# Kernel tuning notes

Measured on AMD Instinct MI355X. Metric: run time of the kernel, lower is better.

Reference implementation:

```python
import jax, jax.numpy as jnp
import numpy as np

D = 256
H = 8
HD = D // H
LN_EPS = 1e-5


def setup_inputs() -> dict:
    key = jax.random.key(0)
    ks = jax.random.split(key, 20)
    N = 768
    s = lambda *sh: 1.0 / np.sqrt(sh[-1])
    inp = {
        "features": jax.random.normal(ks[0], (N, D), jnp.float32),
        "boxes": jax.random.uniform(ks[1], (N, 4), jnp.float32),
        # MultiheadAttention params (torch layout: [out, in])
        "in_proj_w": jax.random.normal(ks[2], (3 * D, D), jnp.float32) * s(D),
        "in_proj_b": jnp.zeros((3 * D,), jnp.float32),
        "out_proj_w": jax.random.normal(ks[3], (D, D), jnp.float32) * s(D),
        "out_proj_b": jnp.zeros((D,), jnp.float32),
        # similarity_net params
        "w1": jax.random.normal(ks[4], (256, 3 * D + 3), jnp.float32) * s(3 * D + 3),
        "b1": jnp.zeros((256,), jnp.float32),
        "ln_g": jnp.ones((256,), jnp.float32),
        "ln_b": jnp.zeros((256,), jnp.float32),
        "w2": jax.random.normal(ks[5], (128, 256), jnp.float32) * s(256),
        "b2": jnp.zeros((128,), jnp.float32),
        "w3": jax.random.normal(ks[6], (64, 128), jnp.float32) * s(128),
        "b3": jnp.zeros((64,), jnp.float32),
        "w4": jax.random.normal(ks[7], (32, 64), jnp.float32) * s(64),
        "b4": jnp.zeros((32,), jnp.float32),
        "w5": jax.random.normal(ks[8], (1, 32), jnp.float32) * s(32),
        "b5": jnp.zeros((1,), jnp.float32),
    }
    return inp


def _mha(x, in_w, in_b, out_w, out_b):
    # x: [N, D]; torch nn.MultiheadAttention self-attention (eval mode)
    N = x.shape[0]
    qkv = x @ in_w.T + in_b                      # [N, 3D]
    q, k, v = jnp.split(qkv, 3, axis=-1)
    q = q.reshape(N, H, HD).transpose(1, 0, 2)   # [H, N, HD]
    k = k.reshape(N, H, HD).transpose(1, 0, 2)
    v = v.reshape(N, H, HD).transpose(1, 0, 2)
    scores = jnp.einsum("hnd,hmd->hnm", q, k) / np.sqrt(HD)
    attn = jax.nn.softmax(scores, axis=-1)
    o = jnp.einsum("hnm,hmd->hnd", attn, v)      # [H, N, HD]
    o = o.transpose(1, 0, 2).reshape(N, D)
    return o @ out_w.T + out_b


def reference(features, boxes, in_proj_w, in_proj_b, out_proj_w, out_proj_b,
              w1, b1, ln_g, ln_b, w2, b2, w3, b3, w4, b4, w5, b5):
    N = features.shape[0]
    att = _mha(features, in_proj_w, in_proj_b, out_proj_w, out_proj_b)  # [N, D]

    fi = jnp.broadcast_to(att[:, None, :], (N, N, D))
    fj = jnp.broadcast_to(att[None, :, :], (N, N, D))
    bi = boxes[:, None, :]
    bj = boxes[None, :, :]
    x_dist = jnp.abs(bi[:, :, 0] - bj[:, :, 0])
    y_diff = bi[:, :, 1] - bj[:, :, 1]
    spatial = jnp.stack([x_dist, jnp.abs(y_diff), y_diff], axis=-1)    # [N, N, 3]
    pairs = jnp.concatenate([fi, fj, fi * fj, spatial], axis=-1)       # [N, N, 3D+3]

    h = jax.nn.relu(pairs @ w1.T + b1)
    mu = jnp.mean(h, axis=-1, keepdims=True)
    var = jnp.var(h, axis=-1, keepdims=True)
    h = (h - mu) / jnp.sqrt(var + LN_EPS) * ln_g + ln_b
    h = jax.nn.relu(h @ w2.T + b2)
    h = jax.nn.relu(h @ w3.T + b3)
    h = jax.nn.relu(h @ w4.T + b4)
    logits = (h @ w5.T + b5)[..., 0]                                   # [N, N]

    eye = jnp.eye(N, dtype=logits.dtype)
    return logits * (1.0 - eye) - 1e9 * eye
```

## Files before the change

kernel.cpp:

```cpp
#include <hip/hip_runtime.h>


typedef __attribute__((ext_vector_type(8))) __bf16 bf16x8;
typedef __attribute__((ext_vector_type(4))) float f32x4;

__device__ __forceinline__ float bf2f(unsigned short u) {
    return __uint_as_float(((unsigned int)u) << 16);
}
__device__ __forceinline__ unsigned short f2bf(float f) {
    union { __bf16 b; unsigned short u; } cv;
    cv.b = (__bf16)f;
    return cv.u;
}
__device__ __forceinline__ int pk4_fp8(float a, float b, float c, float d) {
    int w = __builtin_amdgcn_cvt_pk_fp8_f32(a, b, 0, false);
    w = __builtin_amdgcn_cvt_pk_fp8_f32(c, d, w, true);
    return w;
}
__device__ __forceinline__ unsigned char f2fp8(float v) {
    return (unsigned char)(__builtin_amdgcn_cvt_pk_fp8_f32(v, 0.f, 0, false) & 0xff);
}

__global__ __launch_bounds__(256) void pack_all(
    const float* __restrict__ features, const float* __restrict__ in_proj_w,
    const float* __restrict__ out_proj_w, const float* __restrict__ w1,
    const float* __restrict__ w2, const float* __restrict__ w3,
    const float* __restrict__ w4, const float* __restrict__ b1,
    const float* __restrict__ ln_g, const float* __restrict__ ln_b,
    const float* __restrict__ b2, const float* __restrict__ out_proj_b,
    unsigned short* __restrict__ featb, unsigned short* __restrict__ inWb,
    unsigned short* __restrict__ WcatB, unsigned short* __restrict__ outWTb,
    unsigned short* __restrict__ wABb,
    unsigned char* __restrict__ w1c_f8, unsigned char* __restrict__ w2g_f8,
    unsigned char* __restrict__ w3_f8, unsigned char* __restrict__ w4_f8,
    float* __restrict__ bias768, float* __restrict__ c1, float* __restrict__ c2,
    float* __restrict__ biasZ)
{
    int t = blockIdx.x * 256 + threadIdx.x;
    if (t < 196608) {
        featb[t] = f2bf(features[t]);
    } else if (t < 393216) {
        int u = t - 196608; inWb[u] = f2bf(in_proj_w[u]);
    } else if (t < 458752) {
        int u = t - 393216; WcatB[u] = f2bf(out_proj_w[u]);
    } else if (t < 524288) {
        int u = t - 458752; int e = u >> 8, d = u & 255;
        outWTb[u] = f2bf(out_proj_w[d * 256 + e]);
    } else if (t < 655360) {
        int u = t - 524288; int n = u >> 8, k = u & 255;
        float v = (n < 256) ? w1[n * 771 + k] : w1[(n - 256) * 771 + 256 + k];
        wABb[u] = f2bf(v);
    } else if (t < 729088) {
        int u = t - 655360;
        int e = u & 7, lane = (u >> 3) & 63, f = u >> 9;
        int l15 = lane & 15, quad = lane >> 4;
        int mt = f & 15, kc = f >> 4;
        int o = mt * 16 + l15, k = kc * 32 + quad * 8 + e;
        float v;
        if (k < 256)            v = w1[o * 771 + 512 + k];
        else if (k < 259)       v = w1[o * 771 + 768 + (k - 256)];
        else                    v = 0.f;
        w1c_f8[u] = f2fp8(v);
    } else if (t < 761856) {
        int u = t - 729088;
        int e = u & 7, lane = (u >> 3) & 63, f = u >> 9;
        int l15 = lane & 15, quad = lane >> 4;
        int mt = f & 7, kc = f >> 3;
        int o = mt * 16 + l15, k = kc * 32 + quad * 8 + e;
        w2g_f8[u] = f2fp8(w2[o * 256 + k] * ln_g[k]);
    } else if (t < 770048) {
        int u = t - 761856;
        int e = u & 7, lane = (u >> 3) & 63, f = u >> 9;
        int l15 = lane & 15, quad = lane >> 4;
        int mt = f & 3, kc = f >> 2;
        int o = mt * 16 + l15, k = kc * 32 + quad * 8 + e;
        w3_f8[u] = f2fp8(w3[o * 128 + k]);
    } else if (t < 772096) {
        int u = t - 770048;
        int e = u & 7, lane = (u >> 3) & 63, f = u >> 9;
        int l15 = lane & 15, quad = lane >> 4;
        int mt = f & 1, kc = f >> 1;
        int o = mt * 16 + l15, k = kc * 32 + quad * 8 + e;
        w4_f8[u] = f2fp8(w4[o * 64 + k]);
    } else if (t < 772864) {
        int n = t - 772096;
        if (n < 256) bias768[n] = out_proj_b[n];
        else {
            int m = n - 256;
            float s = 0.f;
            for (int d = 0; d < 256; d += 4) {
                float4 ob = *reinterpret_cast<const float4*>(&out_proj_b[d]);
                const float* wr = (m < 256) ? &w1[m * 771 + d]
                                            : &w1[(m - 256) * 771 + 256 + d];
                float4 w = *reinterpret_cast<const float4*>(wr);
                s += ob.x * w.x + ob.y * w.y + ob.z * w.z + ob.w * w.w;
            }
            bias768[n] = s + ((m < 256) ? b1[m] : 0.f);
        }
    } else if (t < 772992) {
        int p = t - 772864;
        float s2 = 0.f, s1 = 0.f;
        for (int k = 0; k < 256; k += 4) {
            float4 w = *reinterpret_cast<const float4*>(&w2[p * 256 + k]);
            float4 g = *reinterpret_cast<const float4*>(&ln_g[k]);
            float4 lb = *reinterpret_cast<const float4*>(&ln_b[k]);
            s2 += g.x * w.x + g.y * w.y + g.z * w.z + g.w * w.w;
            s1 += lb.x * w.x + lb.y * w.y + lb.z * w.z + lb.w * w.w;
        }
        c2[p] = s2;
        c1[p] = s1 + b2[p];
    } else if (t < 773248) {
        biasZ[t - 772992] = 0.f;
    }
}

__global__ __launch_bounds__(256) void gemm_bf(
    const unsigned short* __restrict__ A, const unsigned short* __restrict__ W,
    const float* __restrict__ bias, float* __restrict__ Cf,
    unsigned short* __restrict__ Cbf, unsigned short* __restrict__ Vt,
    int N, int K, int ldc, int tcol0)
{
    const int wv = threadIdx.x >> 6, lane = threadIdx.x & 63;
    const int l15 = lane & 15, quad = lane >> 4;
    const int row0 = blockIdx.x * 64 + wv * 16;
    const int col0 = blockIdx.y * 64;
    f32x4 acc[4] = {};
    for (int kc = 0; kc < (K >> 5); ++kc) {
        bf16x8 a = *reinterpret_cast<const bf16x8*>(&A[(row0 + l15) * K + kc * 32 + quad * 8]);
#pragma unroll
        for (int ct = 0; ct < 4; ++ct) {
            bf16x8 b = *reinterpret_cast<const bf16x8*>(&W[(col0 + ct * 16 + l15) * K + kc * 32 + quad * 8]);
            acc[ct] = __builtin_amdgcn_mfma_f32_16x16x32_bf16(a, b, acc[ct], 0, 0, 0);
        }
    }
#pragma unroll
    for (int ct = 0; ct < 4; ++ct)
#pragma unroll
        for (int r = 0; r < 4; ++r) {
            int row = row0 + quad * 4 + r, col = col0 + ct * 16 + l15;
            float v = acc[ct][r] + bias[col];
            if (Vt && col >= tcol0) {
                Vt[(col - tcol0) * 768 + row] = f2bf(v);
            } else {
                if (Cf)  Cf[row * ldc + col] = v;
                if (Cbf) Cbf[row * ldc + col] = f2bf(v);
            }
        }
}

__global__ __launch_bounds__(256) void gemm_attab(
    const unsigned short* __restrict__ A, const unsigned short* __restrict__ W,
    const float* __restrict__ bias, float* __restrict__ att,
    unsigned short* __restrict__ attb, float* __restrict__ AB)
{
    const int wv = threadIdx.x >> 6, lane = threadIdx.x & 63;
    const int l15 = lane & 15, quad = lane >> 4;
    const int row0 = blockIdx.x * 64 + wv * 16;
    const int col0 = blockIdx.y * 64;
    f32x4 acc[4] = {};
    for (int kc = 0; kc < 8; ++kc) {
        bf16x8 a = *reinterpret_cast<const bf16x8*>(&A[(row0 + l15) * 256 + kc * 32 + quad * 8]);
#pragma unroll
        for (int ct = 0; ct < 4; ++ct) {
            bf16x8 b = *reinterpret_cast<const bf16x8*>(&W[(col0 + ct * 16 + l15) * 256 + kc * 32 + quad * 8]);
            acc[ct] = __builtin_amdgcn_mfma_f32_16x16x32_bf16(a, b, acc[ct], 0, 0, 0);
        }
    }
#pragma unroll
    for (int ct = 0; ct < 4; ++ct)
#pragma unroll
        for (int r = 0; r < 4; ++r) {
            int row = row0 + quad * 4 + r, col = col0 + ct * 16 + l15;
            float v = acc[ct][r] + bias[col];
            if (col < 256) {
                att[row * 256 + col] = v;
                attb[row * 256 + col] = f2bf(v);
            } else {
                AB[row * 512 + (col - 256)] = v;
            }
        }
}

#define SP 776

__global__ __launch_bounds__(256) void attn_mfma(
    const unsigned short* __restrict__ qkvb, const unsigned short* __restrict__ Vt,
    unsigned short* __restrict__ Obf)
{
    __shared__ __align__(16) unsigned short smS[64 * SP];
    const int h = blockIdx.x, q0 = blockIdx.y * 64, hb = h * 32;
    const int tid = threadIdx.x, wave = tid >> 6, lane = tid & 63;
    const int l15 = lane & 15, quad = lane >> 4;

    bf16x8 af[4];
#pragma unroll
    for (int mt = 0; mt < 4; ++mt)
        af[mt] = *reinterpret_cast<const bf16x8*>(&qkvb[(q0 + mt * 16 + l15) * 768 + hb + quad * 8]);
#pragma unroll
    for (int ct = 0; ct < 12; ++ct) {
        int n0 = wave * 192 + ct * 16;
        bf16x8 b = *reinterpret_cast<const bf16x8*>(&qkvb[(n0 + l15) * 768 + 256 + hb + quad * 8]);
#pragma unroll
        for (int mt = 0; mt < 4; ++mt) {
            f32x4 c = {};
            c = __builtin_amdgcn_mfma_f32_16x16x32_bf16(af[mt], b, c, 0, 0, 0);
#pragma unroll
            for (int r = 0; r < 4; ++r)
                smS[(mt * 16 + quad * 4 + r) * SP + n0 + l15] =
                    f2bf(c[r] * 0.17677669529663689f);
        }
    }
    __syncthreads();

    {
        const int row = tid >> 2, part = tid & 3;
        unsigned short* rp = &smS[row * SP + part * 192];
        float mx = -3.0e38f;
#pragma unroll
        for (int c8 = 0; c8 < 24; ++c8) {
            uint4 v = *reinterpret_cast<const uint4*>(&rp[c8 * 8]);
            const unsigned short* pe = reinterpret_cast<const unsigned short*>(&v);
#pragma unroll
            for (int e = 0; e < 8; ++e) mx = fmaxf(mx, bf2f(pe[e]));
        }
        mx = fmaxf(mx, __shfl_xor(mx, 1, 64));
        mx = fmaxf(mx, __shfl_xor(mx, 2, 64));
        float ls = 0.f;
#pragma unroll
        for (int c8 = 0; c8 < 24; ++c8) {
            uint4 v = *reinterpret_cast<const uint4*>(&rp[c8 * 8]);
            const unsigned short* pe = reinterpret_cast<const unsigned short*>(&v);
            unsigned short o8[8];
#pragma unroll
            for (int e = 0; e < 8; ++e) {
                float ev = __expf(bf2f(pe[e]) - mx);
                ls += ev;
                o8[e] = f2bf(ev);
            }
            *reinterpret_cast<uint4*>(&rp[c8 * 8]) = *reinterpret_cast<const uint4*>(o8);
        }
        ls += __shfl_xor(ls, 1, 64);
        ls += __shfl_xor(ls, 2, 64);
        float inv = 1.0f / ls;
#pragma unroll
        for (int c8 = 0; c8 < 24; ++c8) {
            uint4 v = *reinterpret_cast<const uint4*>(&rp[c8 * 8]);
            const unsigned short* pe = reinterpret_cast<const unsigned short*>(&v);
            unsigned short o8[8];
#pragma unroll
            for (int e = 0; e < 8; ++e) o8[e] = f2bf(bf2f(pe[e]) * inv);
            *reinterpret_cast<uint4*>(&rp[c8 * 8]) = *reinterpret_cast<const uint4*>(o8);
        }
    }
    f32x4 accp[2] = {};
    for (int kc = 0; kc < 24; ++kc) {
        bf16x8 a = *reinterpret_cast<const bf16x8*>(&smS[(wave * 16 + l15) * SP + kc * 32 + quad * 8]);
#pragma unroll
        for (int ct = 0; ct < 2; ++ct) {
            bf16x8 b = *reinterpret_cast<const bf16x8*>(&Vt[(hb + ct * 16 + l15) * 768 + kc * 32 + quad * 8]);
            accp[ct] = __builtin_amdgcn_mfma_f32_16x16x32_bf16(a, b, accp[ct], 0, 0, 0);
        }
    }
#pragma unroll
    for (int ct = 0; ct < 2; ++ct)
#pragma unroll
        for (int r = 0; r < 4; ++r) {
            int row = q0 + wave * 16 + quad * 4 + r;
            Obf[row * 256 + hb + ct * 16 + l15] = f2bf(accp[ct][r]);
        }
}

#define S1 296
#define S2 136
#define S3 72

__global__ __launch_bounds__(256, 4) void pair_mlp(
    const float* __restrict__ att, const unsigned short* __restrict__ attb,
    const float* __restrict__ AB,
    const unsigned char* __restrict__ w1c_f8, const unsigned char* __restrict__ w2g_f8,
    const unsigned char* __restrict__ w3_f8, const unsigned char* __restrict__ w4_f8,
    const float* __restrict__ boxes,
    const float* __restrict__ c1, const float* __restrict__ c2,
    const float* __restrict__ b3, const float* __restrict__ b4,
    const float* __restrict__ w5, const float* __restrict__ b5,
    float* __restrict__ out)
{
    __shared__ __align__(16) unsigned char smH[64 * S1];
    __shared__ float s_psum[64][4], s_pssq[64][4];
    __shared__ float s_mu[64], s_rs[64];
    __shared__ float s_l5[64][2];

    const int i    = blockIdx.x;
    const int j0   = blockIdx.y * 64;
    const int tid  = threadIdx.x;
    const int wave = tid >> 6;
    const int lane = tid & 63;
    const int l15  = lane & 15;
    const int quad = lane >> 4;

    {
        const int g = tid & 63;
        float4 fi4 = *reinterpret_cast<const float4*>(&att[i * 256 + g * 4]);
#pragma unroll
        for (int it = 0; it < 16; ++it) {
            int r = (tid >> 6) + it * 4;
            uint2 aj = *reinterpret_cast<const uint2*>(&attb[(j0 + r) * 256 + g * 4]);
            float a0 = __uint_as_float(aj.x << 16);
            float a1 = __uint_as_float(aj.x & 0xffff0000u);
            float a2 = __uint_as_float(aj.y << 16);
            float a3 = __uint_as_float(aj.y & 0xffff0000u);
            *reinterpret_cast<int*>(&smH[r * S1 + g * 4]) =
                pk4_fp8(a0 * fi4.x, a1 * fi4.y, a2 * fi4.z, a3 * fi4.w);
        }
    }
    if (tid < 64) {
        int j = j0 + tid;
        float xd = fabsf(boxes[i * 4 + 0] - boxes[j * 4 + 0]);
        float yd = boxes[i * 4 + 1] - boxes[j * 4 + 1];
        *reinterpret_cast<int*>(&smH[tid * S1 + 256]) = pk4_fp8(xd, fabsf(yd), yd, 0.f);
        *reinterpret_cast<int*>(&smH[tid * S1 + 260]) = 0;
        *reinterpret_cast<long long*>(&smH[tid * S1 + 264]) = 0;
        *reinterpret_cast<long long*>(&smH[tid * S1 + 272]) = 0;
        *reinterpret_cast<long long*>(&smH[tid * S1 + 280]) = 0;
    }
    __syncthreads();

    f32x4 acc1[4][4] = {};
    for (int kc = 0; kc < 9; ++kc) {
        long long a[4];
#pragma unroll
        for (int mt = 0; mt < 4; ++mt)
            a[mt] = *reinterpret_cast<const long long*>(&w1c_f8[((kc * 16 + wave * 4 + mt) * 64 + lane) * 8]);
#pragma unroll
        for (int nt = 0; nt < 4; ++nt) {
            long long b = *reinterpret_cast<const long long*>(&smH[(nt * 16 + l15) * S1 + kc * 32 + quad * 8]);
#pragma unroll
            for (int mt = 0; mt < 4; ++mt)
                acc1[mt][nt] = __builtin_amdgcn_mfma_f32_16x16x32_fp8_fp8(a[mt], b, acc1[mt][nt], 0, 0, 0);
        }
    }

    const int o0 = wave * 64;
    float vsum[4] = {}, vssq[4] = {};
#pragma unroll
    for (int mt = 0; mt < 4; ++mt) {
        int o = o0 + mt * 16 + quad * 4;
        float4 Ai = *reinterpret_cast<const float4*>(&AB[i * 512 + o]);
        float AiA[4] = {Ai.x, Ai.y, Ai.z, Ai.w};
#pragma unroll
        for (int nt = 0; nt < 4; ++nt) {
            int j = nt * 16 + l15;
            float4 Bj = *reinterpret_cast<const float4*>(&AB[(j0 + j) * 512 + 256 + o]);
            float BjA[4] = {Bj.x, Bj.y, Bj.z, Bj.w};
#pragma unroll
            for (int r = 0; r < 4; ++r) {
                float v = fmaxf(acc1[mt][nt][r] + AiA[r] + BjA[r], 0.f);
                acc1[mt][nt][r] = v;
                vsum[nt] += v; vssq[nt] += v * v;
            }
        }
    }
#pragma unroll
    for (int nt = 0; nt < 4; ++nt) {
        vsum[nt] += __shfl_xor(vsum[nt], 16, 64);
        vsum[nt] += __shfl_xor(vsum[nt], 32, 64);
        vssq[nt] += __shfl_xor(vssq[nt], 16, 64);
        vssq[nt] += __shfl_xor(vssq[nt], 32, 64);
    }
    if (quad == 0)
#pragma unroll
        for (int nt = 0; nt < 4; ++nt) {
            s_psum[nt * 16 + l15][wave] = vsum[nt];
            s_pssq[nt * 16 + l15][wave] = vssq[nt];
        }
    __syncthreads();
#pragma unroll
    for (int mt = 0; mt < 4; ++mt) {
        int o = o0 + mt * 16 + quad * 4;
#pragma unroll
        for (int nt = 0; nt < 4; ++nt) {
            int j = nt * 16 + l15;
            *reinterpret_cast<int*>(&smH[j * S1 + o]) =
                pk4_fp8(acc1[mt][nt][0], acc1[mt][nt][1], acc1[mt][nt][2], acc1[mt][nt][3]);
        }
    }
    if (wave == 0) {
        int j = lane;
        float sm = (s_psum[j][0] + s_psum[j][1] + s_psum[j][2] + s_psum[j][3]) * (1.0f / 256.0f);
        float sq = (s_pssq[j][0] + s_pssq[j][1] + s_pssq[j][2] + s_pssq[j][3]) * (1.0f / 256.0f);
        s_mu[j] = sm;
        s_rs[j] = rsqrtf(sq - sm * sm + 1e-5f);
    }
    __syncthreads();

    f32x4 acc2[2][4] = {};
    for (int kc = 0; kc < 8; ++kc) {
        long long a[2];
#pragma unroll
        for (int mt = 0; mt < 2; ++mt)
            a[mt] = *reinterpret_cast<const long long*>(&w2g_f8[((kc * 8 + wave * 2 + mt) * 64 + lane) * 8]);
#pragma unroll
        for (int nt = 0; nt < 4; ++nt) {
            long long b = *reinterpret_cast<const long long*>(&smH[(nt * 16 + l15) * S1 + kc * 32 + quad * 8]);
#pragma unroll
            for (int mt = 0; mt < 2; ++mt)
                acc2[mt][nt] = __builtin_amdgcn_mfma_f32_16x16x32_fp8_fp8(a[mt], b, acc2[mt][nt], 0, 0, 0);
        }
    }
    __syncthreads();
#pragma unroll
    for (int mt = 0; mt < 2; ++mt) {
        int p = wave * 32 + mt * 16 + quad * 4;
        float4 C1 = *reinterpret_cast<const float4*>(&c1[p]);
        float4 C2 = *reinterpret_cast<const float4*>(&c2[p]);
        float C1A[4] = {C1.x, C1.y, C1.z, C1.w};
        float C2A[4] = {C2.x, C2.y, C2.z, C2.w};
#pragma unroll
        for (int nt = 0; nt < 4; ++nt) {
            int j = nt * 16 + l15;
            float mu = s_mu[j], rs = s_rs[j];
            float vv[4];
#pragma unroll
            for (int r = 0; r < 4; ++r)
                vv[r] = fmaxf(rs * (acc2[mt][nt][r] - mu * C2A[r]) + C1A[r], 0.f);
            *reinterpret_cast<int*>(&smH[j * S2 + p]) = pk4_fp8(vv[0], vv[1], vv[2], vv[3]);
        }
    }
    __syncthreads();

    f32x4 acc3[4] = {};
    for (int kc = 0; kc < 4; ++kc) {
        long long a = *reinterpret_cast<const long long*>(&w3_f8[((kc * 4 + wave) * 64 + lane) * 8]);
#pragma unroll
        for (int nt = 0; nt < 4; ++nt) {
            long long b = *reinterpret_cast<const long long*>(&smH[(nt * 16 + l15) * S2 + kc * 32 + quad * 8]);
            acc3[nt] = __builtin_amdgcn_mfma_f32_16x16x32_fp8_fp8(a, b, acc3[nt], 0, 0, 0);
        }
    }
    __syncthreads();
    {
        int q = wave * 16 + quad * 4;
        float4 B3 = *reinterpret_cast<const float4*>(&b3[q]);
        float B3A[4] = {B3.x, B3.y, B3.z, B3.w};
#pragma unroll
        for (int nt = 0; nt < 4; ++nt) {
            int j = nt * 16 + l15;
            float vv[4];
#pragma unroll
            for (int r = 0; r < 4; ++r)
                vv[r] = fmaxf(acc3[nt][r] + B3A[r], 0.f);
            *reinterpret_cast<int*>(&smH[j * S3 + q]) = pk4_fp8(vv[0], vv[1], vv[2], vv[3]);
        }
    }
    __syncthreads();

    const int mt4 = wave & 1;
    const int jh  = wave >> 1;
    f32x4 acc4[2] = {};
#pragma unroll
    for (int kc = 0; kc < 2; ++kc) {
        long long a = *reinterpret_cast<const long long*>(&w4_f8[((kc * 2 + mt4) * 64 + lane) * 8]);
#pragma unroll
        for (int nt = 0; nt < 2; ++nt) {
            int j = jh * 32 + nt * 16 + l15;
            long long b = *reinterpret_cast<const long long*>(&smH[j * S3 + kc * 32 + quad * 8]);
            acc4[nt] = __builtin_amdgcn_mfma_f32_16x16x32_fp8_fp8(a, b, acc4[nt], 0, 0, 0);
        }
    }
    {
        int o4 = mt4 * 16 + quad * 4;
        float4 B4 = *reinterpret_cast<const float4*>(&b4[o4]);
        float4 W5 = *reinterpret_cast<const float4*>(&w5[o4]);
        float B4A[4] = {B4.x, B4.y, B4.z, B4.w};
        float W5A[4] = {W5.x, W5.y, W5.z, W5.w};
#pragma unroll
        for (int nt = 0; nt < 2; ++nt) {
            float part = 0.f;
#pragma unroll
            for (int r = 0; r < 4; ++r)
                part += fmaxf(acc4[nt][r] + B4A[r], 0.f) * W5A[r];
            part += __shfl_xor(part, 16, 64);
            part += __shfl_xor(part, 32, 64);
            if (quad == 0)
                s_l5[jh * 32 + nt * 16 + l15][mt4] = part;
        }
    }
    __syncthreads();
    if (tid < 64) {
        int j = j0 + tid;
        float v = s_l5[tid][0] + s_l5[tid][1] + b5[0];
        out[i * 768 + j] = (j == i) ? -1.0e9f : v;
    }
}

extern "C" void kernel_launch(void* const* d_in, const int* in_sizes, int n_in,
                              void* d_out, int out_size, void* d_ws, size_t ws_size,
                              hipStream_t stream)
{
    const float* features   = (const float*)d_in[0];
    const float* boxes      = (const float*)d_in[1];
    const float* in_proj_w  = (const float*)d_in[2];
    const float* in_proj_b  = (const float*)d_in[3];
    const float* out_proj_w = (const float*)d_in[4];
    const float* out_proj_b = (const float*)d_in[5];
    const float* w1  = (const float*)d_in[6];
    const float* b1  = (const float*)d_in[7];
    const float* ln_g = (const float*)d_in[8];
    const float* ln_b = (const float*)d_in[9];
    const float* w2  = (const float*)d_in[10];
    const float* b2  = (const float*)d_in[11];
    const float* w3  = (const float*)d_in[12];
    const float* b3  = (const float*)d_in[13];
    const float* w4  = (const float*)d_in[14];
    const float* b4  = (const float*)d_in[15];
    const float* w5  = (const float*)d_in[16];
    const float* b5  = (const float*)d_in[17];
    float* out = (float*)d_out;

    char* p = (char*)d_ws;
    unsigned short* qkvb  = (unsigned short*)p; p += 768 * 768 * 2;
    unsigned short* Vt    = (unsigned short*)p; p += 256 * 768 * 2;
    unsigned short* Obf   = (unsigned short*)p; p += 768 * 256 * 2;
    unsigned short* attb  = (unsigned short*)p; p += 768 * 256 * 2;
    float* att = (float*)p; p += 768 * 256 * 4;
    float* AB  = (float*)p; p += 768 * 512 * 4;
    unsigned short* featb  = (unsigned short*)p; p += 196608 * 2;
    unsigned short* inWb   = (unsigned short*)p; p += 196608 * 2;
    unsigned short* WcatB  = (unsigned short*)p; p += 196608 * 2;
    unsigned short* outWTb = (unsigned short*)p; p += 65536 * 2;
    unsigned short* wABb   = (unsigned short*)p; p += 131072 * 2;
    unsigned char* w1c_f8  = (unsigned char*)p; p += 73728;
    unsigned char* w2g_f8  = (unsigned char*)p; p += 32768;
    unsigned char* w3_f8   = (unsigned char*)p; p += 8192;
    unsigned char* w4_f8   = (unsigned char*)p; p += 2048;
    float* bias768 = (float*)p; p += 768 * 4;
    float* c1v     = (float*)p; p += 128 * 4;
    float* c2v     = (float*)p; p += 128 * 4;
    float* biasZ   = (float*)p; p += 256 * 4;

    pack_all<<<dim3(3021), dim3(256), 0, stream>>>(features, in_proj_w,
        out_proj_w, w1, w2, w3, w4, b1, ln_g, ln_b, b2, out_proj_b,
        featb, inWb, WcatB, outWTb, wABb, w1c_f8, w2g_f8, w3_f8, w4_f8,
        bias768, c1v, c2v, biasZ);
    gemm_bf<<<dim3(8, 4), dim3(256), 0, stream>>>(wABb, outWTb, biasZ,
        (float*)nullptr, WcatB + 65536, (unsigned short*)nullptr, 256, 256, 256, 1 << 30);
    gemm_bf<<<dim3(12, 12), dim3(256), 0, stream>>>(featb, inWb, in_proj_b,
        (float*)nullptr, qkvb, Vt, 768, 256, 768, 512);
    attn_mfma<<<dim3(8, 12), dim3(256), 0, stream>>>(qkvb, Vt, Obf);
    gemm_attab<<<dim3(12, 12), dim3(256), 0, stream>>>(Obf, WcatB, bias768,
        att, attb, AB);
    pair_mlp<<<dim3(768, 12), dim3(256), 0, stream>>>(att, attb, AB,
        w1c_f8, w2g_f8, w3_f8, w4_f8, boxes, c1v, c2v,
        b3, b4, w5, b5, out);
}
```

Baseline: 304.7 us.

## Use 32x32x16 fp8 MFMA for pair MLP layers 1-2 and split attention blocks

The first two pair-MLP GEMMs move from 16x16x32 to 32x32x16 fp8 MFMA instructions, and the w1/w2 fp8 weight packing is re-laid out to match the 32-row fragment layout. The goal is fewer MFMA issues and fewer LDS B-fragment loads per output. Layers 2 and 3 now get their own shared buffers (smH2, smH3), which removes one barrier at the cost of extra LDS per block, and that may lower occupancy. Attention blocks are halved to 32 query rows, doubling the grid so more CUs are busy, with an added barrier before the PV product.

```diff
diff --git a/kernel.cpp b/kernel.cpp
--- a/kernel.cpp
+++ b/kernel.cpp
@@ -3,6 +3,7 @@
 
 typedef __attribute__((ext_vector_type(8))) __bf16 bf16x8;
 typedef __attribute__((ext_vector_type(4))) float f32x4;
+typedef __attribute__((ext_vector_type(16))) float f32x16;
 
 __device__ __forceinline__ float bf2f(unsigned short u) {
     return __uint_as_float(((unsigned int)u) << 16);
@@ -53,9 +54,9 @@
     } else if (t < 729088) {
         int u = t - 655360;
         int e = u & 7, lane = (u >> 3) & 63, f = u >> 9;
-        int l15 = lane & 15, quad = lane >> 4;
-        int mt = f & 15, kc = f >> 4;
-        int o = mt * 16 + l15, k = kc * 32 + quad * 8 + e;
+        int ot = f & 7, k16 = f >> 3;
+        int o = ot * 32 + (lane & 31);
+        int k = k16 * 16 + ((lane >> 5) & 1) * 8 + e;
         float v;
         if (k < 256)            v = w1[o * 771 + 512 + k];
         else if (k < 259)       v = w1[o * 771 + 768 + (k - 256)];
@@ -64,10 +65,10 @@
     } else if (t < 761856) {
         int u = t - 729088;
         int e = u & 7, lane = (u >> 3) & 63, f = u >> 9;
-        int l15 = lane & 15, quad = lane >> 4;
-        int mt = f & 7, kc = f >> 3;
-        int o = mt * 16 + l15, k = kc * 32 + quad * 8 + e;
-        w2g_f8[u] = f2fp8(w2[o * 256 + k] * ln_g[k]);
+        int pt = f & 3, k16 = f >> 2;
+        int p = pt * 32 + (lane & 31);
+        int k = k16 * 16 + ((lane >> 5) & 1) * 8 + e;
+        w2g_f8[u] = f2fp8(w2[p * 256 + k] * ln_g[k]);
     } else if (t < 770048) {
         int u = t - 761856;
         int e = u & 7, lane = (u >> 3) & 63, f = u >> 9;
@@ -187,21 +188,21 @@
     const unsigned short* __restrict__ qkvb, const unsigned short* __restrict__ Vt,
     unsigned short* __restrict__ Obf)
 {
-    __shared__ __align__(16) unsigned short smS[64 * SP];
-    const int h = blockIdx.x, q0 = blockIdx.y * 64, hb = h * 32;
+    __shared__ __align__(16) unsigned short smS[32 * SP];
+    const int h = blockIdx.x, q0 = blockIdx.y * 32, hb = h * 32;
     const int tid = threadIdx.x, wave = tid >> 6, lane = tid & 63;
     const int l15 = lane & 15, quad = lane >> 4;
 
-    bf16x8 af[4];
-#pragma unroll
-    for (int mt = 0; mt < 4; ++mt)
+    bf16x8 af[2];
+#pragma unroll
+    for (int mt = 0; mt < 2; ++mt)
         af[mt] = *reinterpret_cast<const bf16x8*>(&qkvb[(q0 + mt * 16 + l15) * 768 + hb + quad * 8]);
 #pragma unroll
     for (int ct = 0; ct < 12; ++ct) {
         int n0 = wave * 192 + ct * 16;
         bf16x8 b = *reinterpret_cast<const bf16x8*>(&qkvb[(n0 + l15) * 768 + 256 + hb + quad * 8]);
 #pragma unroll
-        for (int mt = 0; mt < 4; ++mt) {
+        for (int mt = 0; mt < 2; ++mt) {
             f32x4 c = {};
             c = __builtin_amdgcn_mfma_f32_16x16x32_bf16(af[mt], b, c, 0, 0, 0);
 #pragma unroll
@@ -213,11 +214,11 @@
     __syncthreads();
 
     {
-        const int row = tid >> 2, part = tid & 3;
-        unsigned short* rp = &smS[row * SP + part * 192];
+        const int row = tid >> 3, part = tid & 7;
+        unsigned short* rp = &smS[row * SP + part * 96];
         float mx = -3.0e38f;
 #pragma unroll
-        for (int c8 = 0; c8 < 24; ++c8) {
+        for (int c8 = 0; c8 < 12; ++c8) {
             uint4 v = *reinterpret_cast<const uint4*>(&rp[c8 * 8]);
             const unsigned short* pe = reinterpret_cast<const unsigned short*>(&v);
 #pragma unroll
@@ -225,9 +226,10 @@
         }
         mx = fmaxf(mx, __shfl_xor(mx, 1, 64));
         mx = fmaxf(mx, __shfl_xor(mx, 2, 64));
+        mx = fmaxf(mx, __shfl_xor(mx, 4, 64));
         float ls = 0.f;
 #pragma unroll
-        for (int c8 = 0; c8 < 24; ++c8) {
+        for (int c8 = 0; c8 < 12; ++c8) {
             uint4 v = *reinterpret_cast<const uint4*>(&rp[c8 * 8]);
             const unsigned short* pe = reinterpret_cast<const unsigned short*>(&v);
             unsigned short o8[8];
@@ -241,9 +243,10 @@
         }
         ls += __shfl_xor(ls, 1, 64);
         ls += __shfl_xor(ls, 2, 64);
+        ls += __shfl_xor(ls, 4, 64);
         float inv = 1.0f / ls;
 #pragma unroll
-        for (int c8 = 0; c8 < 24; ++c8) {
+        for (int c8 = 0; c8 < 12; ++c8) {
             uint4 v = *reinterpret_cast<const uint4*>(&rp[c8 * 8]);
             const unsigned short* pe = reinterpret_cast<const unsigned short*>(&v);
             unsigned short o8[8];
@@ -252,22 +255,20 @@
             *reinterpret_cast<uint4*>(&rp[c8 * 8]) = *reinterpret_cast<const uint4*>(o8);
         }
     }
-    f32x4 accp[2] = {};
+    __syncthreads();
+
+    const int row0 = (wave >> 1) * 16, cg = wave & 1;
+    f32x4 accp = {};
     for (int kc = 0; kc < 24; ++kc) {
-        bf16x8 a = *reinterpret_cast<const bf16x8*>(&smS[(wave * 16 + l15) * SP + kc * 32 + quad * 8]);
-#pragma unroll
-        for (int ct = 0; ct < 2; ++ct) {
-            bf16x8 b = *reinterpret_cast<const bf16x8*>(&Vt[(hb + ct * 16 + l15) * 768 + kc * 32 + quad * 8]);
-            accp[ct] = __builtin_amdgcn_mfma_f32_16x16x32_bf16(a, b, accp[ct], 0, 0, 0);
-        }
-    }
-#pragma unroll
-    for (int ct = 0; ct < 2; ++ct)
-#pragma unroll
-        for (int r = 0; r < 4; ++r) {
-            int row = q0 + wave * 16 + quad * 4 + r;
-            Obf[row * 256 + hb + ct * 16 + l15] = f2bf(accp[ct][r]);
-        }
+        bf16x8 a = *reinterpret_cast<const bf16x8*>(&smS[(row0 + l15) * SP + kc * 32 + quad * 8]);
+        bf16x8 b = *reinterpret_cast<const bf16x8*>(&Vt[(hb + cg * 16 + l15) * 768 + kc * 32 + quad * 8]);
+        accp = __builtin_amdgcn_mfma_f32_16x16x32_bf16(a, b, accp, 0, 0, 0);
+    }
+#pragma unroll
+    for (int r = 0; r < 4; ++r) {
+        int row = q0 + row0 + quad * 4 + r;
+        Obf[row * 256 + hb + cg * 16 + l15] = f2bf(accp[r]);
+    }
 }
 
 #define S1 296
@@ -286,6 +287,8 @@
     float* __restrict__ out)
 {
     __shared__ __align__(16) unsigned char smH[64 * S1];
+    __shared__ __align__(16) unsigned char smH2[64 * S2];
+    __shared__ __align__(16) unsigned char smH3[64 * S3];
     __shared__ float s_psum[64][4], s_pssq[64][4];
     __shared__ float s_mu[64], s_rs[64];
     __shared__ float s_l5[64][2];
@@ -297,6 +300,8 @@
     const int lane = tid & 63;
     const int l15  = lane & 15;
     const int quad = lane >> 4;
+    const int l31  = lane & 31;
+    const int half = lane >> 5;
 
     {
         const int g = tid & 63;
@@ -325,65 +330,65 @@
     }
     __syncthreads();
 
-    f32x4 acc1[4][4] = {};
-    for (int kc = 0; kc < 9; ++kc) {
-        long long a[4];
-#pragma unroll
-        for (int mt = 0; mt < 4; ++mt)
-            a[mt] = *reinterpret_cast<const long long*>(&w1c_f8[((kc * 16 + wave * 4 + mt) * 64 + lane) * 8]);
-#pragma unroll
-        for (int nt = 0; nt < 4; ++nt) {
-            long long b = *reinterpret_cast<const long long*>(&smH[(nt * 16 + l15) * S1 + kc * 32 + quad * 8]);
-#pragma unroll
-            for (int mt = 0; mt < 4; ++mt)
-                acc1[mt][nt] = __builtin_amdgcn_mfma_f32_16x16x32_fp8_fp8(a[mt], b, acc1[mt][nt], 0, 0, 0);
+    f32x16 acc1[2][2] = {};
+    for (int k16 = 0; k16 < 18; ++k16) {
+        long long a0 = *reinterpret_cast<const long long*>(&w1c_f8[((k16 * 8 + wave * 2 + 0) * 64 + lane) * 8]);
+        long long a1 = *reinterpret_cast<const long long*>(&w1c_f8[((k16 * 8 + wave * 2 + 1) * 64 + lane) * 8]);
+#pragma unroll
+        for (int jt = 0; jt < 2; ++jt) {
+            long long b = *reinterpret_cast<const long long*>(&smH[(jt * 32 + l31) * S1 + k16 * 16 + half * 8]);
+            acc1[0][jt] = __builtin_amdgcn_mfma_f32_32x32x16_fp8_fp8(a0, b, acc1[0][jt], 0, 0, 0);
+            acc1[1][jt] = __builtin_amdgcn_mfma_f32_32x32x16_fp8_fp8(a1, b, acc1[1][jt], 0, 0, 0);
         }
     }
 
     const int o0 = wave * 64;
-    float vsum[4] = {}, vssq[4] = {};
-#pragma unroll
-    for (int mt = 0; mt < 4; ++mt) {
-        int o = o0 + mt * 16 + quad * 4;
-        float4 Ai = *reinterpret_cast<const float4*>(&AB[i * 512 + o]);
-        float AiA[4] = {Ai.x, Ai.y, Ai.z, Ai.w};
-#pragma unroll
-        for (int nt = 0; nt < 4; ++nt) {
-            int j = nt * 16 + l15;
-            float4 Bj = *reinterpret_cast<const float4*>(&AB[(j0 + j) * 512 + 256 + o]);
-            float BjA[4] = {Bj.x, Bj.y, Bj.z, Bj.w};
-#pragma unroll
-            for (int r = 0; r < 4; ++r) {
-                float v = fmaxf(acc1[mt][nt][r] + AiA[r] + BjA[r], 0.f);
-                acc1[mt][nt][r] = v;
-                vsum[nt] += v; vssq[nt] += v * v;
+    float vsum[2] = {}, vssq[2] = {};
+#pragma unroll
+    for (int ot = 0; ot < 2; ++ot)
+#pragma unroll
+        for (int q4 = 0; q4 < 4; ++q4) {
+            int ob = o0 + ot * 32 + q4 * 8 + half * 4;
+            float4 Ai = *reinterpret_cast<const float4*>(&AB[i * 512 + ob]);
+            float AiA[4] = {Ai.x, Ai.y, Ai.z, Ai.w};
+#pragma unroll
+            for (int jt = 0; jt < 2; ++jt) {
+                int j = jt * 32 + l31;
+                float4 Bj = *reinterpret_cast<const float4*>(&AB[(j0 + j) * 512 + 256 + ob]);
+                float BjA[4] = {Bj.x, Bj.y, Bj.z, Bj.w};
+#pragma unroll
+                for (int r = 0; r < 4; ++r) {
+                    float v = fmaxf(acc1[ot][jt][q4 * 4 + r] + AiA[r] + BjA[r], 0.f);
+                    acc1[ot][jt][q4 * 4 + r] = v;
+                    vsum[jt] += v; vssq[jt] += v * v;
+                }
             }
         }
-    }
-#pragma unroll
-    for (int nt = 0; nt < 4; ++nt) {
-        vsum[nt] += __shfl_xor(vsum[nt], 16, 64);
-        vsum[nt] += __shfl_xor(vsum[nt], 32, 64);
-        vssq[nt] += __shfl_xor(vssq[nt], 16, 64);
-        vssq[nt] += __shfl_xor(vssq[nt], 32, 64);
-    }
-    if (quad == 0)
-#pragma unroll
-        for (int nt = 0; nt < 4; ++nt) {
-            s_psum[nt * 16 + l15][wave] = vsum[nt];
-            s_pssq[nt * 16 + l15][wave] = vssq[nt];
-        }
-    __syncthreads();
-#pragma unroll
-    for (int mt = 0; mt < 4; ++mt) {
-        int o = o0 + mt * 16 + quad * 4;
-#pragma unroll
-        for (int nt = 0; nt < 4; ++nt) {
-            int j = nt * 16 + l15;
-            *reinterpret_cast<int*>(&smH[j * S1 + o]) =
-                pk4_fp8(acc1[mt][nt][0], acc1[mt][nt][1], acc1[mt][nt][2], acc1[mt][nt][3]);
-        }
-    }
+#pragma unroll
+    for (int jt = 0; jt < 2; ++jt) {
+        vsum[jt] += __shfl_xor(vsum[jt], 32, 64);
+        vssq[jt] += __shfl_xor(vssq[jt], 32, 64);
+    }
+    if (half == 0)
+#pragma unroll
+        for (int jt = 0; jt < 2; ++jt) {
+            s_psum[jt * 32 + l31][wave] = vsum[jt];
+            s_pssq[jt * 32 + l31][wave] = vssq[jt];
+        }
+    __syncthreads();
+#pragma unroll
+    for (int ot = 0; ot < 2; ++ot)
+#pragma unroll
+        for (int q4 = 0; q4 < 4; ++q4) {
+            int ob = o0 + ot * 32 + q4 * 8 + half * 4;
+#pragma unroll
+            for (int jt = 0; jt < 2; ++jt) {
+                int j = jt * 32 + l31;
+                *reinterpret_cast<int*>(&smH[j * S1 + ob]) =
+                    pk4_fp8(acc1[ot][jt][q4 * 4 + 0], acc1[ot][jt][q4 * 4 + 1],
+                            acc1[ot][jt][q4 * 4 + 2], acc1[ot][jt][q4 * 4 + 3]);
+            }
+        }
     if (wave == 0) {
         int j = lane;
         float sm = (s_psum[j][0] + s_psum[j][1] + s_psum[j][2] + s_psum[j][3]) * (1.0f / 256.0f);
@@ -393,37 +398,31 @@
     }
     __syncthreads();
 
-    f32x4 acc2[2][4] = {};
-    for (int kc = 0; kc < 8; ++kc) {
-        long long a[2];
-#pragma unroll
-        for (int mt = 0; mt < 2; ++mt)
-            a[mt] = *reinterpret_cast<const long long*>(&w2g_f8[((kc * 8 + wave * 2 + mt) * 64 + lane) * 8]);
-#pragma unroll
-        for (int nt = 0; nt < 4; ++nt) {
-            long long b = *reinterpret_cast<const long long*>(&smH[(nt * 16 + l15) * S1 + kc * 32 + quad * 8]);
-#pragma unroll
-            for (int mt = 0; mt < 2; ++mt)
-                acc2[mt][nt] = __builtin_amdgcn_mfma_f32_16x16x32_fp8_fp8(a[mt], b, acc2[mt][nt], 0, 0, 0);
-        }
-    }
-    __syncthreads();
-#pragma unroll
-    for (int mt = 0; mt < 2; ++mt) {
-        int p = wave * 32 + mt * 16 + quad * 4;
-        float4 C1 = *reinterpret_cast<const float4*>(&c1[p]);
-        float4 C2 = *reinterpret_cast<const float4*>(&c2[p]);
+    f32x16 acc2[2] = {};
+    for (int k16 = 0; k16 < 16; ++k16) {
+        long long a = *reinterpret_cast<const long long*>(&w2g_f8[((k16 * 4 + wave) * 64 + lane) * 8]);
+#pragma unroll
+        for (int jt = 0; jt < 2; ++jt) {
+            long long b = *reinterpret_cast<const long long*>(&smH[(jt * 32 + l31) * S1 + k16 * 16 + half * 8]);
+            acc2[jt] = __builtin_amdgcn_mfma_f32_32x32x16_fp8_fp8(a, b, acc2[jt], 0, 0, 0);
+        }
+    }
+#pragma unroll
+    for (int q4 = 0; q4 < 4; ++q4) {
+        int pb = wave * 32 + q4 * 8 + half * 4;
+        float4 C1 = *reinterpret_cast<const float4*>(&c1[pb]);
+        float4 C2 = *reinterpret_cast<const float4*>(&c2[pb]);
         float C1A[4] = {C1.x, C1.y, C1.z, C1.w};
         float C2A[4] = {C2.x, C2.y, C2.z, C2.w};
 #pragma unroll
-        for (int nt = 0; nt < 4; ++nt) {
-            int j = nt * 16 + l15;
+        for (int jt = 0; jt < 2; ++jt) {
+            int j = jt * 32 + l31;
             float mu = s_mu[j], rs = s_rs[j];
             float vv[4];
 #pragma unroll
             for (int r = 0; r < 4; ++r)
-                vv[r] = fmaxf(rs * (acc2[mt][nt][r] - mu * C2A[r]) + C1A[r], 0.f);
-            *reinterpret_cast<int*>(&smH[j * S2 + p]) = pk4_fp8(vv[0], vv[1], vv[2], vv[3]);
+                vv[r] = fmaxf(rs * (acc2[jt][q4 * 4 + r] - mu * C2A[r]) + C1A[r], 0.f);
+            *reinterpret_cast<int*>(&smH2[j * S2 + pb]) = pk4_fp8(vv[0], vv[1], vv[2], vv[3]);
         }
     }
     __syncthreads();
@@ -433,11 +432,10 @@
         long long a = *reinterpret_cast<const long long*>(&w3_f8[((kc * 4 + wave) * 64 + lane) * 8]);
 #pragma unroll
         for (int nt = 0; nt < 4; ++nt) {
-            long long b = *reinterpret_cast<const long long*>(&smH[(nt * 16 + l15) * S2 + kc * 32 + quad * 8]);
+            long long b = *reinterpret_cast<const long long*>(&smH2[(nt * 16 + l15) * S2 + kc * 32 + quad * 8]);
             acc3[nt] = __builtin_amdgcn_mfma_f32_16x16x32_fp8_fp8(a, b, acc3[nt], 0, 0, 0);
         }
     }
-    __syncthreads();
     {
         int q = wave * 16 + quad * 4;
         float4 B3 = *reinterpret_cast<const float4*>(&b3[q]);
@@ -449,7 +447,7 @@
 #pragma unroll
             for (int r = 0; r < 4; ++r)
                 vv[r] = fmaxf(acc3[nt][r] + B3A[r], 0.f);
-            *reinterpret_cast<int*>(&smH[j * S3 + q]) = pk4_fp8(vv[0], vv[1], vv[2], vv[3]);
+            *reinterpret_cast<int*>(&smH3[j * S3 + q]) = pk4_fp8(vv[0], vv[1], vv[2], vv[3]);
         }
     }
     __syncthreads();
@@ -463,7 +461,7 @@
 #pragma unroll
         for (int nt = 0; nt < 2; ++nt) {
             int j = jh * 32 + nt * 16 + l15;
-            long long b = *reinterpret_cast<const long long*>(&smH[j * S3 + kc * 32 + quad * 8]);
+            long long b = *reinterpret_cast<const long long*>(&smH3[j * S3 + kc * 32 + quad * 8]);
             acc4[nt] = __builtin_amdgcn_mfma_f32_16x16x32_fp8_fp8(a, b, acc4[nt], 0, 0, 0);
         }
     }
@@ -546,7 +544,7 @@
         (float*)nullptr, WcatB + 65536, (unsigned short*)nullptr, 256, 256, 256, 1 << 30);
     gemm_bf<<<dim3(12, 12), dim3(256), 0, stream>>>(featb, inWb, in_proj_b,
         (float*)nullptr, qkvb, Vt, 768, 256, 768, 512);
-    attn_mfma<<<dim3(8, 12), dim3(256), 0, stream>>>(qkvb, Vt, Obf);
+    attn_mfma<<<dim3(8, 24), dim3(256), 0, stream>>>(qkvb, Vt, Obf);
     gemm_attab<<<dim3(12, 12), dim3(256), 0, stream>>>(Obf, WcatB, bias768,
         att, attb, AB);
     pair_mlp<<<dim3(768, 12), dim3(256), 0, stream>>>(att, attb, AB,
```

New measurement: 303.3 us. No clear change (-0.5%).
